# Optimization experiments

Measured on AMD Instinct MI355X. Metric: run time of the kernel, lower is better.

## Reference

```python
import jax, jax.numpy as jnp
import numpy as np


def setup_inputs() -> dict:
    key = jax.random.key(0)
    k1, k2, k3, k4 = jax.random.split(key, 4)
    B, S, H, I, E = 2, 2048, 2048, 1024, 8
    return {
        "hidden_states": jax.random.normal(k1, (B, S, H), dtype=jnp.float32),
        "gate_w": jax.random.normal(k2, (E, H), dtype=jnp.float32) * 0.02,
        "gate_up_weight": jax.random.normal(k3, (H, 2 * I), dtype=jnp.float32)[None].repeat(E, 0) * 0.0
        + jax.random.normal(k3, (E, H, 2 * I), dtype=jnp.float32) * 0.1,
        "down_weight": jax.random.normal(k4, (E, I, H), dtype=jnp.float32) * 0.1,
    }


def reference(hidden_states, gate_w, gate_up_weight, down_weight):
    B, S, H = hidden_states.shape
    E = gate_w.shape[0]
    I = down_weight.shape[1]
    x = hidden_states.reshape(-1, H)                       # [T, H]
    router_logits = x @ gate_w.T                           # [T, E]
    # top-1 routing: selected expert keeps sigmoid(logit), others sigmoid(-inf)=0
    selected = jnp.argmax(router_logits, axis=-1)          # [T]
    onehot = jax.nn.one_hot(selected, E, dtype=router_logits.dtype)  # [T, E]
    routing = jax.nn.sigmoid(router_logits) * onehot       # [T, E]
    # INPUT-side routing: replicate input per expert, scale, then dense BMMs
    batched_input = routing.T[:, :, None] * x[None]        # [E, T, H]
    gate_up = jnp.einsum("eth,ehf->etf", batched_input, gate_up_weight)  # [E, T, 2I]
    up, gate = gate_up[..., :I], gate_up[..., I:]
    activated = up * jax.nn.silu(gate)                     # [E, T, I]
    out = jnp.einsum("eti,eih->eth", activated, down_weight)  # [E, T, H]
    out = out.sum(axis=0)                                  # [T, H]
    return out.reshape(B, S, H)
```

## Files before the change

### kernel.cpp

```cpp
#include <hip/hip_runtime.h>
#include <hip/hip_bf16.h>
#include <cstddef>
#include <cstdint>

#define T_TOK 4096
#define H_DIM 2048
#define E_NUM 8
#define I_DIM 1024
#define TWO_I 2048
#define MROWS 5120
#define MT    40

typedef __attribute__((ext_vector_type(8))) short bf16x8;
typedef __attribute__((ext_vector_type(4))) float f32x4;
typedef __attribute__((ext_vector_type(4))) int   i32x4;

#define WS_SCALE   0
#define WS_COUNTS  16384
#define WS_BUCKETS 18432
#define WS_SLOTTOK 149504
#define WS_XSG     (1u<<20)
#define WS_ACT     22020096u
#define WS_W1T     32505856u
#define WS_W2T     99614720u

__device__ __forceinline__ short f2bf(float f) {
    uint32_t u = __builtin_bit_cast(uint32_t, f);
    u += 0x7fffu + ((u >> 16) & 1u);
    return (short)(u >> 16);
}

__device__ __forceinline__ void gload16(const void* g, void* l) {
    __builtin_amdgcn_global_load_lds(
        (const __attribute__((address_space(1))) void*)g,
        (__attribute__((address_space(3))) void*)l, 16, 0, 0);
}

__device__ __forceinline__ uint32_t cvt_pk_bf16(float lo, float hi) {
    uint32_t r;
    asm("v_cvt_pk_bf16_f32 %0, %1, %2" : "=v"(r) : "v"(lo), "v"(hi));
    return r;
}

__device__ __forceinline__ void tcvt_body(
    const float* __restrict__ src, short* __restrict__ dst,
    int K, int e, int k0, int n0)
{
    const int N = TWO_I;
    const int t  = threadIdx.x;
    const int tn = t & 15;
    const int tk = t >> 4;
    const int kk = k0 + tk * 4;
    const int nn = n0 + tn * 4;

    const float* S = src + ((size_t)e * K + kk) * N + nn;
    float4 v0 = *(const float4*)(S);
    float4 v1 = *(const float4*)(S + N);
    float4 v2 = *(const float4*)(S + 2 * N);
    float4 v3 = *(const float4*)(S + 3 * N);

    short* D = dst + ((size_t)e * N + nn) * K + kk;
    uint2 o;
    o.x = cvt_pk_bf16(v0.x, v1.x); o.y = cvt_pk_bf16(v2.x, v3.x);
    *(uint2*)(D) = o;
    o.x = cvt_pk_bf16(v0.y, v1.y); o.y = cvt_pk_bf16(v2.y, v3.y);
    *(uint2*)(D + K) = o;
    o.x = cvt_pk_bf16(v0.z, v1.z); o.y = cvt_pk_bf16(v2.z, v3.z);
    *(uint2*)(D + 2 * K) = o;
    o.x = cvt_pk_bf16(v0.w, v1.w); o.y = cvt_pk_bf16(v2.w, v3.w);
    *(uint2*)(D + 3 * K) = o;
}

__device__ __forceinline__ void router_body(
    int blk, const float* __restrict__ x, const float* __restrict__ gw,
    float* __restrict__ scale, int* __restrict__ counts, int* __restrict__ buckets)
{
    const int wid  = threadIdx.x >> 6;
    const int lane = threadIdx.x & 63;
    const int t = blk * 4 + wid;
    if (t >= T_TOK) return;

    float4 a4[E_NUM];
#pragma unroll
    for (int e = 0; e < E_NUM; ++e) a4[e] = make_float4(0.f, 0.f, 0.f, 0.f);

    const float4* xr  = (const float4*)(x + (size_t)t * H_DIM);
    const float4* gwv = (const float4*)gw;
#pragma unroll
    for (int it = 0; it < 8; ++it) {
        const int idx = lane + it * 64;
        float4 xv = xr[idx];
#pragma unroll
        for (int e = 0; e < E_NUM; ++e) {
            float4 wv = gwv[e * 512 + idx];
            a4[e].x = fmaf(xv.x, wv.x, a4[e].x);
            a4[e].y = fmaf(xv.y, wv.y, a4[e].y);
            a4[e].z = fmaf(xv.z, wv.z, a4[e].z);
            a4[e].w = fmaf(xv.w, wv.w, a4[e].w);
        }
    }
    float acc[E_NUM];
#pragma unroll
    for (int e = 0; e < E_NUM; ++e) {
        float v = (a4[e].x + a4[e].y) + (a4[e].z + a4[e].w);
#pragma unroll
        for (int off = 32; off > 0; off >>= 1) v += __shfl_xor(v, off);
        acc[e] = v;
    }
    if (lane == 0) {
        int best = 0; float bv = acc[0];
#pragma unroll
        for (int e = 1; e < E_NUM; ++e) { if (acc[e] > bv) { bv = acc[e]; best = e; } }
        scale[t] = 1.f / (1.f + expf(-bv));
        int pos = atomicAdd(&counts[best << 5], 1);
        buckets[best * T_TOK + pos] = t;
    }
}

__global__ __launch_bounds__(256) void prep_kernel(
    const float* __restrict__ x, const float* __restrict__ gw,
    const float* __restrict__ gup,
    float* __restrict__ scale, int* __restrict__ counts,
    int* __restrict__ buckets, short* __restrict__ w1t)
{
    const int b = blockIdx.x;
    if (b < 1024) { router_body(b, x, gw, scale, counts, buckets); return; }

    const int idx = b - 1024;
    tcvt_body(gup, w1t, H_DIM, idx >> 10, (idx & 31) * 64, ((idx >> 5) & 31) * 64);
}

__global__ __launch_bounds__(256) void gather_kernel(
    const float* __restrict__ x, const float* __restrict__ scale,
    const int* __restrict__ counts, const int* __restrict__ buckets,
    short* __restrict__ xsg, int* __restrict__ slot_tok,
    const float* __restrict__ dw, short* __restrict__ w2t)
{
    const int b = blockIdx.x;
    if (b >= MROWS) {
        const int idx = b - MROWS;
        tcvt_body(dw, w2t, I_DIM, idx >> 9, (idx & 15) * 64, ((idx >> 4) & 31) * 64);
        return;
    }

    const int r = b;
    int run = 0, eSel = 0, pos = 0;
    bool valid = false;
#pragma unroll
    for (int k = 0; k < E_NUM; ++k) {
        const int c  = counts[k << 5];
        const int cp = (c + 127) & ~127;
        if (r >= run && r < run + cp) { eSel = k; pos = r - run; valid = (pos < c); }
        run += cp;
    }
    const int tok = valid ? buckets[eSel * T_TOK + pos] : -1;
    if (threadIdx.x == 0) slot_tok[r] = tok;

    short* orow = xsg + (size_t)r * H_DIM + threadIdx.x * 8;
    if (!valid) {
        i32x4 z = {0, 0, 0, 0};
        *(i32x4*)orow = z;
        return;
    }
    const float sc = scale[tok];
    const float* xr = x + (size_t)tok * H_DIM + threadIdx.x * 8;
    float4 a = *(const float4*)xr;
    float4 c4 = *(const float4*)(xr + 4);
    short o[8] __attribute__((aligned(16)));
    o[0] = f2bf(a.x * sc);  o[1] = f2bf(a.y * sc);
    o[2] = f2bf(a.z * sc);  o[3] = f2bf(a.w * sc);
    o[4] = f2bf(c4.x * sc); o[5] = f2bf(c4.y * sc);
    o[6] = f2bf(c4.z * sc); o[7] = f2bf(c4.w * sc);
    *(i32x4*)orow = *(const i32x4*)o;
}

__global__ __launch_bounds__(256) void gemm1_mfma_kernel(
    const short* __restrict__ xsg, const short* __restrict__ w1t,
    const int* __restrict__ counts, short* __restrict__ act)
{
    __shared__ short sA[2][128 * 32];
    __shared__ short sB[2][128 * 32];

    const int bid = blockIdx.x;
    const int wg  = (bid & 7) * 80 + (bid >> 3);
    const int nt  = wg / MT;
    const int mt  = wg - nt * MT;
    const int m0  = mt << 7;
    const int f0  = nt << 6;

    int run = 0, e = 0;
#pragma unroll
    for (int k = 0; k < E_NUM; ++k) {
        if (m0 >= run) e = k;
        run += (counts[k << 5] + 127) & ~127;
    }
    if (m0 >= run) return;

    const int tid = threadIdx.x, lane = tid & 63, w = tid >> 6;
    const int g = lane & 3, lr = lane >> 2;
    const int rA0 = (2 * w) * 16 + lr, rA1 = rA0 + 16;

    const short* srcA0 = xsg + (size_t)(m0 + rA0) * H_DIM + g * 8;
    const short* srcA1 = xsg + (size_t)(m0 + rA1) * H_DIM + g * 8;
    const int n0r = (rA0 < 64) ? (f0 + rA0) : (I_DIM + f0 + (rA0 & 63));
    const int n1r = (rA1 < 64) ? (f0 + rA1) : (I_DIM + f0 + (rA1 & 63));
    const short* srcB0 = w1t + ((size_t)e * TWO_I + n0r) * H_DIM + g * 8;
    const short* srcB1 = w1t + ((size_t)e * TWO_I + n1r) * H_DIM + g * 8;

    const int lm = lane & 15, lg8 = (lane >> 4) * 8;
    const int offA = (w * 32 + lm) * 32 + lg8;
    const int offB = lm * 32 + lg8;

    f32x4 acc[2][8];
#pragma unroll
    for (int i = 0; i < 2; ++i)
#pragma unroll
        for (int j = 0; j < 8; ++j) acc[i][j] = (f32x4){0.f, 0.f, 0.f, 0.f};

    auto STG = [&](int buf, int kb) {
        gload16(srcA0 + kb, &sA[buf][(2 * w) * 512]);
        gload16(srcA1 + kb, &sA[buf][(2 * w + 1) * 512]);
        gload16(srcB0 + kb, &sB[buf][(2 * w) * 512]);
        gload16(srcB1 + kb, &sB[buf][(2 * w + 1) * 512]);
    };
    auto CMP = [&](int buf) {
        const short* pA = &sA[buf][offA];
        const short* pB = &sB[buf][offB];
        bf16x8 a0 = *(const bf16x8*)pA;
        bf16x8 a1 = *(const bf16x8*)(pA + 512);
#pragma unroll
        for (int nf = 0; nf < 8; ++nf) {
            bf16x8 b = *(const bf16x8*)(pB + nf * 512);
            acc[0][nf] = __builtin_amdgcn_mfma_f32_16x16x32_bf16(a0, b, acc[0][nf], 0, 0, 0);
            acc[1][nf] = __builtin_amdgcn_mfma_f32_16x16x32_bf16(a1, b, acc[1][nf], 0, 0, 0);
        }
    };

    int cur = 0;
    STG(0, 0);
    for (int kb = 32; kb < H_DIM; kb += 32) {
        __syncthreads();
        STG(cur ^ 1, kb);
        CMP(cur);
        cur ^= 1;
    }
    __syncthreads();
    CMP(cur);

    const int rbase = w * 32 + (lane >> 4) * 4;
#pragma unroll
    for (int mi = 0; mi < 2; ++mi) {
#pragma unroll
        for (int rr = 0; rr < 4; ++rr) {
            const int row = rbase + mi * 16 + rr;
            short* orow = act + (size_t)(m0 + row) * I_DIM + f0 + lm;
#pragma unroll
            for (int nf = 0; nf < 4; ++nf) {
                float up = acc[mi][nf][rr];
                float gt = acc[mi][nf + 4][rr];
                float v  = up * gt / (1.f + expf(-gt));
                orow[nf * 16] = f2bf(v);
            }
        }
    }
}

__global__ __launch_bounds__(256) void gemm2_mfma_kernel(
    const short* __restrict__ actm, const short* __restrict__ w2t,
    const int* __restrict__ counts, const int* __restrict__ slot_tok,
    float* __restrict__ out)
{
    __shared__ short sA[2][128 * 32];
    __shared__ short sB[2][128 * 32];
    __shared__ int   sTok[128];

    const int bid = blockIdx.x;
    const int wg  = (bid & 7) * 80 + (bid >> 3);
    const int nt  = wg / MT;
    const int mt  = wg - nt * MT;
    const int m0  = mt << 7;
    const int h0  = nt << 7;

    int run = 0, e = 0;
#pragma unroll
    for (int k = 0; k < E_NUM; ++k) {
        if (m0 >= run) e = k;
        run += (counts[k << 5] + 127) & ~127;
    }
    if (m0 >= run) return;

    const int tid = threadIdx.x, lane = tid & 63, w = tid >> 6;
    if (tid < 128) sTok[tid] = slot_tok[m0 + tid];

    const int g = lane & 3, lr = lane >> 2;
    const int rA0 = (2 * w) * 16 + lr, rA1 = rA0 + 16;

    const short* srcA0 = actm + (size_t)(m0 + rA0) * I_DIM + g * 8;
    const short* srcA1 = actm + (size_t)(m0 + rA1) * I_DIM + g * 8;
    const short* srcB0 = w2t + ((size_t)e * H_DIM + h0 + rA0) * I_DIM + g * 8;
    const short* srcB1 = w2t + ((size_t)e * H_DIM + h0 + rA1) * I_DIM + g * 8;

    const int lm = lane & 15, lg8 = (lane >> 4) * 8;
    const int offA = (w * 32 + lm) * 32 + lg8;
    const int offB = lm * 32 + lg8;

    f32x4 acc[2][8];
#pragma unroll
    for (int i = 0; i < 2; ++i)
#pragma unroll
        for (int j = 0; j < 8; ++j) acc[i][j] = (f32x4){0.f, 0.f, 0.f, 0.f};

    auto STG = [&](int buf, int kb) {
        gload16(srcA0 + kb, &sA[buf][(2 * w) * 512]);
        gload16(srcA1 + kb, &sA[buf][(2 * w + 1) * 512]);
        gload16(srcB0 + kb, &sB[buf][(2 * w) * 512]);
        gload16(srcB1 + kb, &sB[buf][(2 * w + 1) * 512]);
    };
    auto CMP = [&](int buf) {
        const short* pA = &sA[buf][offA];
        const short* pB = &sB[buf][offB];
        bf16x8 a0 = *(const bf16x8*)pA;
        bf16x8 a1 = *(const bf16x8*)(pA + 512);
#pragma unroll
        for (int nf = 0; nf < 8; ++nf) {
            bf16x8 b = *(const bf16x8*)(pB + nf * 512);
            acc[0][nf] = __builtin_amdgcn_mfma_f32_16x16x32_bf16(a0, b, acc[0][nf], 0, 0, 0);
            acc[1][nf] = __builtin_amdgcn_mfma_f32_16x16x32_bf16(a1, b, acc[1][nf], 0, 0, 0);
        }
    };

    int cur = 0;
    STG(0, 0);
    for (int kb = 32; kb < I_DIM; kb += 32) {
        __syncthreads();
        STG(cur ^ 1, kb);
        CMP(cur);
        cur ^= 1;
    }
    __syncthreads();
    CMP(cur);

    const int rbase = w * 32 + (lane >> 4) * 4;
#pragma unroll
    for (int mi = 0; mi < 2; ++mi) {
#pragma unroll
        for (int rr = 0; rr < 4; ++rr) {
            const int row = rbase + mi * 16 + rr;
            const int tok = sTok[row];
            if (tok < 0) continue;
            float* orow = out + (size_t)tok * H_DIM + h0 + lm;
#pragma unroll
            for (int nf = 0; nf < 8; ++nf) orow[nf * 16] = acc[mi][nf][rr];
        }
    }
}

extern "C" void kernel_launch(void* const* d_in, const int* in_sizes, int n_in,
                              void* d_out, int out_size, void* d_ws, size_t ws_size,
                              hipStream_t stream) {
    const float* x   = (const float*)d_in[0];
    const float* gw  = (const float*)d_in[1];
    const float* gup = (const float*)d_in[2];
    const float* dw  = (const float*)d_in[3];
    float* out = (float*)d_out;

    char* ws = (char*)d_ws;
    float* scale    = (float*)(ws + WS_SCALE);
    int*   counts   = (int*)(ws + WS_COUNTS);
    int*   buckets  = (int*)(ws + WS_BUCKETS);
    int*   slot_tok = (int*)(ws + WS_SLOTTOK);
    short* xsg      = (short*)(ws + WS_XSG);
    short* act      = (short*)(ws + WS_ACT);
    short* w1t      = (short*)(ws + WS_W1T);
    short* w2t      = (short*)(ws + WS_W2T);

    hipMemsetAsync(counts, 0, 256 * sizeof(int), stream);

    prep_kernel<<<1024 + 8192, 256, 0, stream>>>(
        x, gw, gup, scale, counts, buckets, w1t);

    gather_kernel<<<MROWS + 4096, 256, 0, stream>>>(
        x, scale, counts, buckets, xsg, slot_tok, dw, w2t);

    gemm1_mfma_kernel<<<MT * 16, 256, 0, stream>>>(xsg, w1t, counts, act);
    gemm2_mfma_kernel<<<MT * 16, 256, 0, stream>>>(act, w2t, counts, slot_tok, out);
}
```

Baseline: 204.2 us.

## Triple-buffer GEMM K-loop with vmcnt waits and overlap w2 conversion with gemm1

Both MFMA GEMMs move from a double-buffered K loop with __syncthreads to a three-stage LDS pipeline. Each stage uses explicit s_waitcnt vmcnt counts and raw barriers, so two tile loads stay in flight while one is computed. The down-weight transpose and bf16 conversion blocks move from the gather kernel into extra blocks of the gemm1 launch, so they can fill idle CUs alongside gemm1. The trade-off is more LDS per block and a reliance on hand-counted vmcnt values, which must match the number of loads issued per STG.

```diff
diff --git a/kernel.cpp b/kernel.cpp
--- a/kernel.cpp
+++ b/kernel.cpp
@@ -133,17 +133,9 @@
 __global__ __launch_bounds__(256) void gather_kernel(
     const float* __restrict__ x, const float* __restrict__ scale,
     const int* __restrict__ counts, const int* __restrict__ buckets,
-    short* __restrict__ xsg, int* __restrict__ slot_tok,
-    const float* __restrict__ dw, short* __restrict__ w2t)
-{
-    const int b = blockIdx.x;
-    if (b >= MROWS) {
-        const int idx = b - MROWS;
-        tcvt_body(dw, w2t, I_DIM, idx >> 9, (idx & 15) * 64, ((idx >> 4) & 31) * 64);
-        return;
-    }
-
-    const int r = b;
+    short* __restrict__ xsg, int* __restrict__ slot_tok)
+{
+    const int r = blockIdx.x;
     int run = 0, eSel = 0, pos = 0;
     bool valid = false;
 #pragma unroll
@@ -174,14 +166,39 @@
     *(i32x4*)orow = *(const i32x4*)o;
 }
 
+
+#define GEMM_PIPE(NKT)                                                         \
+    STG(0, 0); STG(1, 32); STG(2, 64);                                         \
+    int cb = 0;                                                                \
+    for (int t = 0; t < (NKT); ++t) {                                          \
+        const int rem = (NKT) - 1 - t;                                         \
+        if (rem >= 2)      asm volatile("s_waitcnt vmcnt(8)" ::: "memory");    \
+        else if (rem == 1) asm volatile("s_waitcnt vmcnt(4)" ::: "memory");    \
+        else               asm volatile("s_waitcnt vmcnt(0)" ::: "memory");    \
+        __builtin_amdgcn_s_barrier();                                          \
+        CMP(cb);                                                               \
+        asm volatile("s_waitcnt lgkmcnt(0)" ::: "memory");                     \
+        __builtin_amdgcn_sched_barrier(0);                                     \
+        __builtin_amdgcn_s_barrier();                                          \
+        if (t + 3 < (NKT)) STG(cb, (t + 3) * 32);                              \
+        cb = (cb == 2) ? 0 : cb + 1;                                           \
+    }
+
 __global__ __launch_bounds__(256) void gemm1_mfma_kernel(
     const short* __restrict__ xsg, const short* __restrict__ w1t,
-    const int* __restrict__ counts, short* __restrict__ act)
-{
-    __shared__ short sA[2][128 * 32];
-    __shared__ short sB[2][128 * 32];
+    const int* __restrict__ counts, short* __restrict__ act,
+    const float* __restrict__ dw, short* __restrict__ w2t)
+{
+    __shared__ short sA[3][4096];
+    __shared__ short sB[3][4096];
 
     const int bid = blockIdx.x;
+    if (bid >= 640) {
+        const int idx = bid - 640;
+        tcvt_body(dw, w2t, I_DIM, idx >> 9, (idx & 15) * 64, ((idx >> 4) & 31) * 64);
+        return;
+    }
+
     const int wg  = (bid & 7) * 80 + (bid >> 3);
     const int nt  = wg / MT;
     const int mt  = wg - nt * MT;
@@ -236,16 +253,7 @@
         }
     };
 
-    int cur = 0;
-    STG(0, 0);
-    for (int kb = 32; kb < H_DIM; kb += 32) {
-        __syncthreads();
-        STG(cur ^ 1, kb);
-        CMP(cur);
-        cur ^= 1;
-    }
-    __syncthreads();
-    CMP(cur);
+    GEMM_PIPE(H_DIM / 32)
 
     const int rbase = w * 32 + (lane >> 4) * 4;
 #pragma unroll
@@ -270,8 +278,8 @@
     const int* __restrict__ counts, const int* __restrict__ slot_tok,
     float* __restrict__ out)
 {
-    __shared__ short sA[2][128 * 32];
-    __shared__ short sB[2][128 * 32];
+    __shared__ short sA[3][4096];
+    __shared__ short sB[3][4096];
     __shared__ int   sTok[128];
 
     const int bid = blockIdx.x;
@@ -329,16 +337,7 @@
         }
     };
 
-    int cur = 0;
-    STG(0, 0);
-    for (int kb = 32; kb < I_DIM; kb += 32) {
-        __syncthreads();
-        STG(cur ^ 1, kb);
-        CMP(cur);
-        cur ^= 1;
-    }
-    __syncthreads();
-    CMP(cur);
+    GEMM_PIPE(I_DIM / 32)
 
     const int rbase = w * 32 + (lane >> 4) * 4;
 #pragma unroll
@@ -379,9 +378,10 @@
     prep_kernel<<<1024 + 8192, 256, 0, stream>>>(
         x, gw, gup, scale, counts, buckets, w1t);
 
-    gather_kernel<<<MROWS + 4096, 256, 0, stream>>>(
-        x, scale, counts, buckets, xsg, slot_tok, dw, w2t);
-
-    gemm1_mfma_kernel<<<MT * 16, 256, 0, stream>>>(xsg, w1t, counts, act);
+    gather_kernel<<<MROWS, 256, 0, stream>>>(
+        x, scale, counts, buckets, xsg, slot_tok);
+
+    gemm1_mfma_kernel<<<640 + 4096, 256, 0, stream>>>(xsg, w1t, counts, act, dw, w2t);
+
     gemm2_mfma_kernel<<<MT * 16, 256, 0, stream>>>(act, w2t, counts, slot_tok, out);
 }
```

New measurement: 176.0 us. -13.8%, faster.
